# Performance work log

Measured on AMD Instinct MI355X. Metric: run time of the kernel, lower is better.

## Reference

```python
import jax, jax.numpy as jnp
import numpy as np

M0, M1, M2 = 128, 64, 32            # multiplicities of 0e, 1o, 2e
NUM_IRREPS = M0 + M1 + M2           # 224
NODE_DIM = 128
SPH_DIM = M0 + 3 * M1 + 5 * M2      # 480
HIDDEN = 2 * NODE_DIM + NUM_IRREPS  # 480
N = 100000
EPS = 1e-5
SQ3 = float(np.sqrt(3.0))
SQ5 = float(np.sqrt(5.0))


def _split(x):
    s0 = x[:, :M0]                                   # [N,128]   l=0
    s1 = x[:, M0:M0 + 3 * M1].reshape(-1, M1, 3)     # [N,64,3]  l=1
    s2 = x[:, M0 + 3 * M1:].reshape(-1, M2, 5)       # [N,32,5]  l=2
    return s0, s1, s2


def _merge(s0, s1, s2):
    n = s0.shape[0]
    return jnp.concatenate([s0, s1.reshape(n, -1), s2.reshape(n, -1)], axis=-1)


def _o3_linear(s0, s1, s2, w0, w1, w2, b0):
    # e3nn o3.Linear: one path per l, element path-normalization 1/sqrt(mul_in); bias only on 0e
    y0 = s0 @ w0 / np.float32(np.sqrt(M0)) + b0
    y1 = jnp.einsum('nik,io->nok', s1, w1) / np.float32(np.sqrt(M1))
    y2 = jnp.einsum('nik,io->nok', s2, w2) / np.float32(np.sqrt(M2))
    return y0, y1, y2


def _o3_layernorm(s0, s1, s2, w, b):
    # equivariant layer norm: mean-center scalars only; RMS over (mul, components) per irrep type
    f0 = s0 - jnp.mean(s0, axis=1, keepdims=True)
    n0 = jnp.mean(f0 * f0, axis=1, keepdims=True)
    f0 = f0 * jax.lax.rsqrt(n0 + EPS) * w[:M0] + b
    n1 = jnp.mean(s1 * s1, axis=(1, 2))[:, None, None]
    f1 = s1 * jax.lax.rsqrt(n1 + EPS) * w[M0:M0 + M1][None, :, None]
    n2 = jnp.mean(s2 * s2, axis=(1, 2))[:, None, None]
    f2 = s2 * jax.lax.rsqrt(n2 + EPS) * w[M0 + M1:][None, :, None]
    return f0, f1, f2


def setup_inputs() -> dict:
    key = jax.random.key(0)
    ks = jax.random.split(key, 16)
    g = lambda k, shape: jax.random.normal(k, shape, jnp.float32)
    return {
        'x_scalar': g(ks[0], (N, NODE_DIM)),
        'x_spherical': g(ks[1], (N, SPH_DIM)),
        'ln_g': jnp.ones((NODE_DIM,), jnp.float32),
        'ln_b': jnp.zeros((NODE_DIM,), jnp.float32),
        'o3n_w': jnp.ones((NUM_IRREPS,), jnp.float32),
        'o3n_b': jnp.zeros((M0,), jnp.float32),
        'U_w0': g(ks[2], (M0, M0)), 'U_w1': g(ks[3], (M1, M1)), 'U_w2': g(ks[4], (M2, M2)),
        'U_b0': jnp.zeros((M0,), jnp.float32),
        'V_w0': g(ks[5], (M0, M0)), 'V_w1': g(ks[6], (M1, M1)), 'V_w2': g(ks[7], (M2, M2)),
        'V_b0': jnp.zeros((M0,), jnp.float32),
        'dot_w': g(ks[8], (NUM_IRREPS, NODE_DIM)) / np.float32(np.sqrt(NUM_IRREPS)),
        'mlp_w1': g(ks[9], (NODE_DIM + NUM_IRREPS, NODE_DIM)) / np.float32(np.sqrt(NODE_DIM + NUM_IRREPS)),
        'mlp_b1': jnp.zeros((NODE_DIM,), jnp.float32),
        'mlp_w2': g(ks[10], (NODE_DIM, HIDDEN)) / np.float32(np.sqrt(NODE_DIM)),
        'mlp_b2': jnp.zeros((HIDDEN,), jnp.float32),
    }


def reference(x_scalar, x_spherical, ln_g, ln_b, o3n_w, o3n_b,
              U_w0, U_w1, U_w2, U_b0, V_w0, V_w1, V_w2, V_b0,
              dot_w, mlp_w1, mlp_b1, mlp_w2, mlp_b2):
    # scalar layer norm
    mu = jnp.mean(x_scalar, axis=-1, keepdims=True)
    var = jnp.var(x_scalar, axis=-1, keepdims=True)
    scalar_in = (x_scalar - mu) * jax.lax.rsqrt(var + EPS) * ln_g + ln_b
    # equivariant layer norm on spherical features
    s0, s1, s2 = _split(x_spherical)
    s0, s1, s2 = _o3_layernorm(s0, s1, s2, o3n_w, o3n_b)
    U0, U1, U2 = _o3_linear(s0, s1, s2, U_w0, U_w1, U_w2, U_b0)
    V0, V1, V2 = _o3_linear(s0, s1, s2, V_w0, V_w1, V_w2, V_b0)
    # o3.Norm: per-irrep L2 norm -> [N, 224]
    inv = jnp.concatenate([jnp.abs(V0),
                           jnp.sqrt(jnp.sum(V1 * V1, axis=-1)),
                           jnp.sqrt(jnp.sum(V2 * V2, axis=-1))], axis=-1)
    mlp_in = jnp.concatenate([scalar_in, inv], axis=-1)          # [N, 352]
    h = jax.nn.silu(mlp_in @ mlp_w1 + mlp_b1)
    mlp_out = h @ mlp_w2 + mlp_b2                                # [N, 480]
    a_vv = mlp_out[:, :NUM_IRREPS]
    a_sv = mlp_out[:, NUM_IRREPS:NUM_IRREPS + NODE_DIM]
    a_ss = mlp_out[:, NUM_IRREPS + NODE_DIM:]
    # ElementwiseTensorProduct with 224x0e: per-irrep scalar gating (net factor 1)
    d0 = U0 * a_vv[:, :M0]
    d1 = U1 * a_vv[:, M0:M0 + M1, None]
    d2 = U2 * a_vv[:, M0 + M1:, None]
    # EquivariantDot (component-normalized uuu TP to 0e): dot / sqrt(2l+1)
    dot = jnp.concatenate([U0 * V0,
                           jnp.sum(U1 * V1, axis=-1) / SQ3,
                           jnp.sum(U2 * V2, axis=-1) / SQ5], axis=-1)
    inner = dot @ dot_w                                           # [N, 128]
    d_scalar = a_sv * inner + a_ss
    return x_scalar + d_scalar, x_spherical + _merge(d0, d1, d2)
```

## Files before the change

kernel.cpp:

```cpp
#include <hip/hip_runtime.h>
#include <stdint.h>

typedef unsigned short u16;
typedef __attribute__((ext_vector_type(4))) unsigned short u16x4;
typedef __attribute__((ext_vector_type(8))) short s16x8;
typedef __attribute__((ext_vector_type(2))) float f32x2;
typedef __attribute__((ext_vector_type(4))) float f32x4;
typedef __attribute__((ext_vector_type(4), aligned(4))) float f32x4u;

#define NROWS 100000
#define RPB   32
#define NBLK  (NROWS / RPB)
#define NTHR  512

#define PF   488
#define PS   360
#define PH   136
#define PD   232
#define PAB  484
#define PIF  132
#define FIN_RG  (16 * PF)
#define SCB_RG  (16 * PS)
#define HB_RG   (16 * PH)
#define DOT_RG  (16 * PD)
#define AOUT_RG (16 * PAB)
#define INN_RG  (16 * PIF)

#define OFF_FIN   0
#define OFF_AOUT  0
#define OFF_SCB   31232
#define OFF_INNER 31232
#define OFF_DOTB  54272
#define OFF_HB    69120
#define OFF_BCOM  77824
#define ARENA_SZ  79552

#define B_UW0 0
#define B_UW1 16384
#define B_UW2 20480
#define B_VW0 21504
#define B_VW1 37888
#define B_VW2 41984
#define B_DW  43008
#define B_W1  71680
#define B_W2  116736
#define PACK_TOT 178176

__device__ inline float bf2f(u16 u) {
    union { uint32_t i; float f; } v; v.i = (uint32_t)u << 16; return v.f;
}
__device__ inline u16 f2bf(float f) {
    uint32_t d; asm("v_cvt_pk_bf16_f32 %0, %1, %1" : "=v"(d) : "v"(f)); return (u16)d;
}
__device__ inline uint32_t cvtpk(float lo, float hi) {
    uint32_t d; asm("v_cvt_pk_bf16_f32 %0, %1, %2" : "=v"(d) : "v"(lo), "v"(hi)); return d;
}
__device__ inline float wsum32(float v) {
    #pragma unroll
    for (int m = 16; m >= 1; m >>= 1) v += __shfl_xor(v, m);
    return v;
}

struct Ptrs {
    const float *xs, *xp, *lng, *lnb, *o3w, *o3b;
    const float *Uw0, *Uw1, *Uw2, *Ub0, *Vw0, *Vw1, *Vw2, *Vb0;
    const float *dw, *w1, *b1, *w2, *b2;
    const u16 *ws;
    float *out;
};

template<int KS, bool PACKED>
__device__ inline void load_b(const void* W, int D, int tile, int lane, s16x8* bfr)
{
    #pragma unroll
    for (int ks = 0; ks < KS; ++ks) {
        if (PACKED) {
            bfr[ks] = *(const s16x8*)((const u16*)W + (((size_t)tile * KS + ks) * 64 + (size_t)lane) * 8);
        } else {
            union { u16 u[8]; s16x8 v; } bb;
            const int k0 = ks * 32 + ((lane >> 4) << 3), o = tile * 16 + (lane & 15);
            #pragma unroll
            for (int j = 0; j < 8; ++j)
                bb.u[j] = f2bf(((const float*)W)[(size_t)(k0 + j) * D + o]);
            bfr[ks] = bb.v;
        }
    }
}

template<int KS>
__device__ inline f32x4 acc_ab(const u16* A, int pitchA, int lane, const s16x8* bfr)
{
    f32x4 acc = {0.f, 0.f, 0.f, 0.f};
    const u16* arow = A + (lane & 15) * pitchA + (lane >> 4) * 8;
    #pragma unroll
    for (int ks = 0; ks < KS; ++ks) {
        s16x8 a = *(const s16x8*)(arow + ks * 32);
        acc = __builtin_amdgcn_mfma_f32_16x16x32_bf16(a, bfr[ks], acc, 0, 0, 0);
    }
    return acc;
}

__global__ void pack_weights(Ptrs P, u16* ws)
{
    const int gid = blockIdx.x * 256 + threadIdx.x;
    if (gid >= PACK_TOT) return;
    const int  base[10] = {B_UW0, B_UW1, B_UW2, B_VW0, B_VW1, B_VW2, B_DW, B_W1, B_W2, PACK_TOT};
    const int  Kd[9]    = {128, 64, 32, 128, 64, 32, 224, 352, 128};
    const float* srcs[9] = {P.Uw0, P.Uw1, P.Uw2, P.Vw0, P.Vw1, P.Vw2, P.dw, P.w1, P.w2};
    const int  Dstride[9] = {128, 64, 32, 128, 64, 32, 128, 128, 480};
    int m = 0;
    for (int i = 1; i < 9; ++i) if (gid >= base[i]) m = i;
    const int e = gid - base[m];
    const int j = e & 7, lane = (e >> 3) & 63, tk = e >> 9;
    const int Ks = Kd[m] >> 5;
    const int ks = tk % Ks, tile = tk / Ks;
    const int k = ks * 32 + ((lane >> 4) << 3) + j;
    const int o = tile * 16 + (lane & 15);
    ws[gid] = f2bf(srcs[m][(size_t)k * Dstride[m] + o]);
}

__device__ inline void stage1_core(const Ptrs& P, u16* fin0, u16* scb0, int tid, int row0)
{
    const int hw = tid >> 5, l32 = tid & 31;
    #pragma unroll
    for (int rg = 0; rg < 2; ++rg) {
        const int rr = hw + rg * 16;
        const size_t row = (size_t)(row0 + rr);
        u16* finr = fin0 + rg * FIN_RG + hw * PF;
        u16* scbr = scb0 + rg * SCB_RG + hw * PS;
        const float* xsf = P.xs + row * 128;
        const float* xpf = P.xp + row * 480;
        {
            f32x4 u = *(const f32x4*)(xsf + l32 * 4);
            float s  = u[0] + u[1] + u[2] + u[3];
            float s2 = u[0]*u[0] + u[1]*u[1] + u[2]*u[2] + u[3]*u[3];
            s = wsum32(s); s2 = wsum32(s2);
            const float mu = s * (1.f / 128.f);
            const float rs = 1.f / sqrtf(s2 * (1.f / 128.f) - mu * mu + 1e-5f);
            const int c = l32 * 4;
            float t[4];
            #pragma unroll
            for (int j2 = 0; j2 < 4; ++j2)
                t[j2] = (u[j2] - mu) * rs * P.lng[c + j2] + P.lnb[c + j2];
            *(uint32_t*)(scbr + c)     = cvtpk(t[0], t[1]);
            *(uint32_t*)(scbr + c + 2) = cvtpk(t[2], t[3]);
        }
        {
            f32x4 u = *(const f32x4*)(xpf + l32 * 4);
            float s  = u[0] + u[1] + u[2] + u[3];
            float s2 = u[0]*u[0] + u[1]*u[1] + u[2]*u[2] + u[3]*u[3];
            s = wsum32(s); s2 = wsum32(s2);
            const float mu = s * (1.f / 128.f);
            const float rs = 1.f / sqrtf(s2 * (1.f / 128.f) - mu * mu + 1e-5f);
            const int c = l32 * 4;
            float t[4];
            #pragma unroll
            for (int j2 = 0; j2 < 4; ++j2)
                t[j2] = (u[j2] - mu) * rs * P.o3w[c + j2] + P.o3b[c + j2];
            *(uint32_t*)(finr + c)     = cvtpk(t[0], t[1]);
            *(uint32_t*)(finr + c + 2) = cvtpk(t[2], t[3]);
        }
        {
            const int cb = l32 * 6;
            f32x4u a = *(const f32x4u*)(xpf + 128 + cb);
            f32x2  b = *(const f32x2*)(xpf + 128 + cb + 4);
            float w[6] = {a[0], a[1], a[2], a[3], b[0], b[1]};
            float ss = 0.f;
            #pragma unroll
            for (int j2 = 0; j2 < 6; ++j2) ss += w[j2] * w[j2];
            ss = wsum32(ss);
            const float rs = 1.f / sqrtf(ss * (1.f / 192.f) + 1e-5f);
            #pragma unroll
            for (int j2 = 0; j2 < 6; ++j2) {
                const int c = cb + j2, i = c / 3, k = c - 3 * i;
                finr[128 + k * 64 + i] = f2bf(w[j2] * rs * P.o3w[128 + i]);
            }
        }
        {
            const int cb = l32 * 5;
            f32x4u a = *(const f32x4u*)(xpf + 320 + cb);
            float w[5] = {a[0], a[1], a[2], a[3], xpf[320 + cb + 4]};
            float ss = 0.f;
            #pragma unroll
            for (int j2 = 0; j2 < 5; ++j2) ss += w[j2] * w[j2];
            ss = wsum32(ss);
            const float rs = 1.f / sqrtf(ss * (1.f / 160.f) + 1e-5f);
            #pragma unroll
            for (int j2 = 0; j2 < 5; ++j2) {
                const int c = cb + j2, i = c / 5, k = c - 5 * i;
                finr[320 + k * 32 + i] = f2bf(w[j2] * rs * P.o3w[192 + i]);
            }
        }
    }
}

template<bool PACKED>
__global__ __launch_bounds__(NTHR, 4) void xpainn_main(Ptrs P)
{
    __shared__ __align__(16) unsigned char arena[ARENA_SZ];
    u16*   fin    = (u16*)(arena + OFF_FIN);
    u16*   aoutB  = (u16*)(arena + OFF_AOUT);
    u16*   scb    = (u16*)(arena + OFF_SCB);
    float* innerF = (float*)(arena + OFF_INNER);
    u16*   dotb   = (u16*)(arena + OFF_DOTB);
    u16*   hb     = (u16*)(arena + OFF_HB);
    u16*   bcom   = (u16*)(arena + OFF_BCOM);

    const int tid = threadIdx.x;
    const int lane = tid & 63, wave = tid >> 6;
    const int r = lane & 15, g = lane >> 4;
    const int row0 = blockIdx.x * RPB;

    for (int i = tid; i < 864; i += NTHR) {
        const float* src; int off;
        if (i < 128)      { src = P.Ub0; off = i; }
        else if (i < 256) { src = P.Vb0; off = i - 128; }
        else if (i < 384) { src = P.b1;  off = i - 256; }
        else              { src = P.b2;  off = i - 384; }
        bcom[i] = f2bf(src[off]);
    }
    stage1_core(P, fin, scb, tid, row0);
    __syncthreads();

    float u0r[2][4];
    float uxr[2][5][4];
    {
        s16x8 bU[4], bV[4];
        load_b<4, PACKED>(PACKED ? (const void*)(P.ws + B_UW0) : (const void*)P.Uw0, 128, wave, lane, bU);
        load_b<4, PACKED>(PACKED ? (const void*)(P.ws + B_VW0) : (const void*)P.Vw0, 128, wave, lane, bV);
        const int o = wave * 16 + r;
        const float bu = bf2f(bcom[o]), bv = bf2f(bcom[128 + o]);
        #pragma unroll
        for (int rg = 0; rg < 2; ++rg) {
            f32x4 au = acc_ab<4>(fin + rg * FIN_RG, PF, lane, bU);
            f32x4 av = acc_ab<4>(fin + rg * FIN_RG, PF, lane, bV);
            u16* scbR = scb + rg * SCB_RG;
            u16* dotR = dotb + rg * DOT_RG;
            #pragma unroll
            for (int q = 0; q < 4; ++q) {
                const float U = au[q] * 0.08838834764831845f + bu;
                const float V = av[q] * 0.08838834764831845f + bv;
                u0r[rg][q] = U;
                const int lrow = g * 4 + q;
                scbR[lrow * PS + 128 + o] = f2bf(fabsf(V));
                dotR[lrow * PD + o]       = f2bf(U * V);
            }
        }
    }
    if (wave < 4) {
        const int tt = wave, o = tt * 16 + r;
        float sv[2][4] = {{0.f,0.f,0.f,0.f},{0.f,0.f,0.f,0.f}};
        float suv[2][4] = {{0.f,0.f,0.f,0.f},{0.f,0.f,0.f,0.f}};
        #pragma unroll
        for (int ch = 0; ch < 3; ++ch) {
            s16x8 bU[2], bV[2];
            load_b<2, PACKED>(PACKED ? (const void*)(P.ws + B_UW1) : (const void*)P.Uw1, 64, tt, lane, bU);
            load_b<2, PACKED>(PACKED ? (const void*)(P.ws + B_VW1) : (const void*)P.Vw1, 64, tt, lane, bV);
            #pragma unroll
            for (int rg = 0; rg < 2; ++rg) {
                f32x4 au = acc_ab<2>(fin + rg * FIN_RG + 128 + 64 * ch, PF, lane, bU);
                f32x4 av = acc_ab<2>(fin + rg * FIN_RG + 128 + 64 * ch, PF, lane, bV);
                #pragma unroll
                for (int q = 0; q < 4; ++q) {
                    const float U = au[q] * 0.125f, V = av[q] * 0.125f;
                    uxr[rg][ch][q] = U; sv[rg][q] += V * V; suv[rg][q] += U * V;
                }
            }
        }
        #pragma unroll
        for (int rg = 0; rg < 2; ++rg) {
            #pragma unroll
            for (int q = 0; q < 4; ++q) {
                const int lrow = g * 4 + q;
                (scb + rg * SCB_RG)[lrow * PS + 256 + o]  = f2bf(sqrtf(sv[rg][q]));
                (dotb + rg * DOT_RG)[lrow * PD + 128 + o] = f2bf(suv[rg][q] * 0.5773502691896258f);
            }
        }
    } else if (wave < 6) {
        const int tt = wave - 4, o = tt * 16 + r;
        float sv[2][4] = {{0.f,0.f,0.f,0.f},{0.f,0.f,0.f,0.f}};
        float suv[2][4] = {{0.f,0.f,0.f,0.f},{0.f,0.f,0.f,0.f}};
        #pragma unroll
        for (int ch = 0; ch < 5; ++ch) {
            s16x8 bU[1], bV[1];
            load_b<1, PACKED>(PACKED ? (const void*)(P.ws + B_UW2) : (const void*)P.Uw2, 32, tt, lane, bU);
            load_b<1, PACKED>(PACKED ? (const void*)(P.ws + B_VW2) : (const void*)P.Vw2, 32, tt, lane, bV);
            #pragma unroll
            for (int rg = 0; rg < 2; ++rg) {
                f32x4 au = acc_ab<1>(fin + rg * FIN_RG + 320 + 32 * ch, PF, lane, bU);
                f32x4 av = acc_ab<1>(fin + rg * FIN_RG + 320 + 32 * ch, PF, lane, bV);
                #pragma unroll
                for (int q = 0; q < 4; ++q) {
                    const float U = au[q] * 0.17677669529663687f, V = av[q] * 0.17677669529663687f;
                    uxr[rg][ch][q] = U; sv[rg][q] += V * V; suv[rg][q] += U * V;
                }
            }
        }
        #pragma unroll
        for (int rg = 0; rg < 2; ++rg) {
            #pragma unroll
            for (int q = 0; q < 4; ++q) {
                const int lrow = g * 4 + q;
                (scb + rg * SCB_RG)[lrow * PS + 320 + o]  = f2bf(sqrtf(sv[rg][q]));
                (dotb + rg * DOT_RG)[lrow * PD + 192 + o] = f2bf(suv[rg][q] * 0.4472135954999579f);
            }
        }
    }
    __syncthreads();

    #pragma unroll
    for (int rg = 0; rg < 2; ++rg) {
        s16x8 bfr[11];
        load_b<11, PACKED>(PACKED ? (const void*)(P.ws + B_W1) : (const void*)P.w1, 128, wave, lane, bfr);
        f32x4 acc = acc_ab<11>(scb + rg * SCB_RG, PS, lane, bfr);
        const int o = wave * 16 + r;
        const float bv = bf2f(bcom[256 + o]);
        #pragma unroll
        for (int q = 0; q < 4; ++q) {
            float x = acc[q] + bv;
            hb[rg * HB_RG + (g * 4 + q) * PH + o] = f2bf(x / (1.f + expf(-x)));
        }
    }
    __syncthreads();

    {
        float avv0[2][4], avv1[2][4];
        {
            s16x8 bfr[4];
            load_b<4, PACKED>(PACKED ? (const void*)(P.ws + B_W2) : (const void*)P.w2, 480, wave, lane, bfr);
            const int o = wave * 16 + r;
            const float bv = bf2f(bcom[384 + o]);
            #pragma unroll
            for (int rg = 0; rg < 2; ++rg) {
                f32x4 acc = acc_ab<4>(hb + rg * HB_RG, PH, lane, bfr);
                #pragma unroll
                for (int q = 0; q < 4; ++q) avv0[rg][q] = acc[q] + bv;
            }
        }
        {
            const int ti = wave + 8;
            s16x8 bfr[4];
            load_b<4, PACKED>(PACKED ? (const void*)(P.ws + B_W2) : (const void*)P.w2, 480, ti, lane, bfr);
            const int o = ti * 16 + r;
            const float bv = bf2f(bcom[384 + o]);
            #pragma unroll
            for (int rg = 0; rg < 2; ++rg) {
                f32x4 acc = acc_ab<4>(hb + rg * HB_RG, PH, lane, bfr);
                if (wave < 6) {
                    #pragma unroll
                    for (int q = 0; q < 4; ++q) avv1[rg][q] = acc[q] + bv;
                } else {
                    u16* aoutR = aoutB + rg * AOUT_RG;
                    #pragma unroll
                    for (int q = 0; q < 4; ++q)
                        aoutR[(g * 4 + q) * PAB + o] = f2bf(acc[q] + bv);
                }
            }
        }
        {
            const size_t ob = (size_t)NROWS * 128;
            #pragma unroll
            for (int rg = 0; rg < 2; ++rg) {
                const int o = wave * 16 + r;
                #pragma unroll
                for (int q = 0; q < 4; ++q) {
                    const size_t gr = (size_t)(row0 + rg * 16 + g * 4 + q) * 480;
                    P.out[ob + gr + o] = P.xp[gr + o] + u0r[rg][q] * avv0[rg][q];
                }
                if (wave < 4) {
                    const int i = wave * 16 + r;
                    #pragma unroll
                    for (int q = 0; q < 4; ++q) {
                        const size_t gr = (size_t)(row0 + rg * 16 + g * 4 + q) * 480;
                        #pragma unroll
                        for (int ch = 0; ch < 3; ++ch) {
                            const size_t c = 128 + 3 * i + ch;
                            P.out[ob + gr + c] = P.xp[gr + c] + uxr[rg][ch][q] * avv1[rg][q];
                        }
                    }
                } else if (wave < 6) {
                    const int i = (wave - 4) * 16 + r;
                    #pragma unroll
                    for (int q = 0; q < 4; ++q) {
                        const size_t gr = (size_t)(row0 + rg * 16 + g * 4 + q) * 480;
                        #pragma unroll
                        for (int ch = 0; ch < 5; ++ch) {
                            const size_t c = 320 + 5 * i + ch;
                            P.out[ob + gr + c] = P.xp[gr + c] + uxr[rg][ch][q] * avv1[rg][q];
                        }
                    }
                }
            }
        }
        for (int ti = wave + 16; ti < 38; ti += 8) {
            if (ti < 30) {
                s16x8 bfr[4];
                load_b<4, PACKED>(PACKED ? (const void*)(P.ws + B_W2) : (const void*)P.w2, 480, ti, lane, bfr);
                const int o = ti * 16 + r;
                const float bv = bf2f(bcom[384 + o]);
                #pragma unroll
                for (int rg = 0; rg < 2; ++rg) {
                    f32x4 acc = acc_ab<4>(hb + rg * HB_RG, PH, lane, bfr);
                    u16* aoutR = aoutB + rg * AOUT_RG;
                    #pragma unroll
                    for (int q = 0; q < 4; ++q)
                        aoutR[(g * 4 + q) * PAB + o] = f2bf(acc[q] + bv);
                }
            } else {
                s16x8 bfr[7];
                load_b<7, PACKED>(PACKED ? (const void*)(P.ws + B_DW) : (const void*)P.dw, 128, ti - 30, lane, bfr);
                const int oo = (ti - 30) * 16 + r;
                #pragma unroll
                for (int rg = 0; rg < 2; ++rg) {
                    f32x4 acc = acc_ab<7>(dotb + rg * DOT_RG, PD, lane, bfr);
                    float* innR = innerF + rg * INN_RG;
                    #pragma unroll
                    for (int q = 0; q < 4; ++q)
                        innR[(g * 4 + q) * PIF + oo] = acc[q];
                }
            }
        }
    }
    __syncthreads();

    #pragma unroll
    for (int it = 0; it < 2; ++it) {
        const int idx = tid + it * NTHR;
        const int r2 = idx >> 5, c4 = (idx & 31) * 4;
        const u16*  aoutR = aoutB + (r2 >> 4) * AOUT_RG + (r2 & 15) * PAB;
        const float* innR = innerF + (r2 >> 4) * INN_RG + (r2 & 15) * PIF;
        const size_t gb = (size_t)(row0 + r2) * 128 + c4;
        const u16x4 asv = *(const u16x4*)(aoutR + 224 + c4);
        const u16x4 ass = *(const u16x4*)(aoutR + 352 + c4);
        const f32x4 inn = *(const f32x4*)(innR + c4);
        const f32x4 xs = *(const f32x4*)(P.xs + gb);
        f32x4 o;
        #pragma unroll
        for (int j = 0; j < 4; ++j) o[j] = xs[j] + bf2f(asv[j]) * inn[j] + bf2f(ass[j]);
        *(f32x4*)(P.out + gb) = o;
    }
}

extern "C" void kernel_launch(void* const* d_in, const int* in_sizes, int n_in,
                              void* d_out, int out_size, void* d_ws, size_t ws_size,
                              hipStream_t stream)
{
    Ptrs P;
    P.xs  = (const float*)d_in[0];  P.xp  = (const float*)d_in[1];
    P.lng = (const float*)d_in[2];  P.lnb = (const float*)d_in[3];
    P.o3w = (const float*)d_in[4];  P.o3b = (const float*)d_in[5];
    P.Uw0 = (const float*)d_in[6];  P.Uw1 = (const float*)d_in[7];
    P.Uw2 = (const float*)d_in[8];  P.Ub0 = (const float*)d_in[9];
    P.Vw0 = (const float*)d_in[10]; P.Vw1 = (const float*)d_in[11];
    P.Vw2 = (const float*)d_in[12]; P.Vb0 = (const float*)d_in[13];
    P.dw  = (const float*)d_in[14]; P.w1  = (const float*)d_in[15];
    P.b1  = (const float*)d_in[16]; P.w2  = (const float*)d_in[17];
    P.b2  = (const float*)d_in[18];
    P.ws  = (const u16*)d_ws;
    P.out = (float*)d_out;

    const bool packed = (ws_size >= (size_t)PACK_TOT * sizeof(u16));
    if (packed) {
        pack_weights<<<(PACK_TOT + 255) / 256, 256, 0, stream>>>(P, (u16*)d_ws);
        xpainn_main<true><<<NBLK, NTHR, 0, stream>>>(P);
    } else {
        xpainn_main<false><<<NBLK, NTHR, 0, stream>>>(P);
    }
}
```

Before: 220.3 us.

## Double block to 1024 threads and redistribute per-stage work across 16 waves

```diff
diff --git a/kernel.cpp b/kernel.cpp
--- a/kernel.cpp
+++ b/kernel.cpp
@@ -11,7 +11,7 @@
 #define NROWS 100000
 #define RPB   32
 #define NBLK  (NROWS / RPB)
-#define NTHR  512
+#define NTHR  1024
 
 #define PF   488
 #define PS   360
@@ -121,81 +121,77 @@
 
 __device__ inline void stage1_core(const Ptrs& P, u16* fin0, u16* scb0, int tid, int row0)
 {
-    const int hw = tid >> 5, l32 = tid & 31;
-    #pragma unroll
-    for (int rg = 0; rg < 2; ++rg) {
-        const int rr = hw + rg * 16;
-        const size_t row = (size_t)(row0 + rr);
-        u16* finr = fin0 + rg * FIN_RG + hw * PF;
-        u16* scbr = scb0 + rg * SCB_RG + hw * PS;
-        const float* xsf = P.xs + row * 128;
-        const float* xpf = P.xp + row * 480;
-        {
-            f32x4 u = *(const f32x4*)(xsf + l32 * 4);
-            float s  = u[0] + u[1] + u[2] + u[3];
-            float s2 = u[0]*u[0] + u[1]*u[1] + u[2]*u[2] + u[3]*u[3];
-            s = wsum32(s); s2 = wsum32(s2);
-            const float mu = s * (1.f / 128.f);
-            const float rs = 1.f / sqrtf(s2 * (1.f / 128.f) - mu * mu + 1e-5f);
-            const int c = l32 * 4;
-            float t[4];
-            #pragma unroll
-            for (int j2 = 0; j2 < 4; ++j2)
-                t[j2] = (u[j2] - mu) * rs * P.lng[c + j2] + P.lnb[c + j2];
-            *(uint32_t*)(scbr + c)     = cvtpk(t[0], t[1]);
-            *(uint32_t*)(scbr + c + 2) = cvtpk(t[2], t[3]);
-        }
-        {
-            f32x4 u = *(const f32x4*)(xpf + l32 * 4);
-            float s  = u[0] + u[1] + u[2] + u[3];
-            float s2 = u[0]*u[0] + u[1]*u[1] + u[2]*u[2] + u[3]*u[3];
-            s = wsum32(s); s2 = wsum32(s2);
-            const float mu = s * (1.f / 128.f);
-            const float rs = 1.f / sqrtf(s2 * (1.f / 128.f) - mu * mu + 1e-5f);
-            const int c = l32 * 4;
-            float t[4];
-            #pragma unroll
-            for (int j2 = 0; j2 < 4; ++j2)
-                t[j2] = (u[j2] - mu) * rs * P.o3w[c + j2] + P.o3b[c + j2];
-            *(uint32_t*)(finr + c)     = cvtpk(t[0], t[1]);
-            *(uint32_t*)(finr + c + 2) = cvtpk(t[2], t[3]);
-        }
-        {
-            const int cb = l32 * 6;
-            f32x4u a = *(const f32x4u*)(xpf + 128 + cb);
-            f32x2  b = *(const f32x2*)(xpf + 128 + cb + 4);
-            float w[6] = {a[0], a[1], a[2], a[3], b[0], b[1]};
-            float ss = 0.f;
-            #pragma unroll
-            for (int j2 = 0; j2 < 6; ++j2) ss += w[j2] * w[j2];
-            ss = wsum32(ss);
-            const float rs = 1.f / sqrtf(ss * (1.f / 192.f) + 1e-5f);
-            #pragma unroll
-            for (int j2 = 0; j2 < 6; ++j2) {
-                const int c = cb + j2, i = c / 3, k = c - 3 * i;
-                finr[128 + k * 64 + i] = f2bf(w[j2] * rs * P.o3w[128 + i]);
-            }
-        }
-        {
-            const int cb = l32 * 5;
-            f32x4u a = *(const f32x4u*)(xpf + 320 + cb);
-            float w[5] = {a[0], a[1], a[2], a[3], xpf[320 + cb + 4]};
-            float ss = 0.f;
-            #pragma unroll
-            for (int j2 = 0; j2 < 5; ++j2) ss += w[j2] * w[j2];
-            ss = wsum32(ss);
-            const float rs = 1.f / sqrtf(ss * (1.f / 160.f) + 1e-5f);
-            #pragma unroll
-            for (int j2 = 0; j2 < 5; ++j2) {
-                const int c = cb + j2, i = c / 5, k = c - 5 * i;
-                finr[320 + k * 32 + i] = f2bf(w[j2] * rs * P.o3w[192 + i]);
-            }
+    const int rr = tid >> 5, l32 = tid & 31;
+    const size_t row = (size_t)(row0 + rr);
+    u16* finr = fin0 + (rr >> 4) * FIN_RG + (rr & 15) * PF;
+    u16* scbr = scb0 + (rr >> 4) * SCB_RG + (rr & 15) * PS;
+    const float* xsf = P.xs + row * 128;
+    const float* xpf = P.xp + row * 480;
+    {
+        f32x4 u = *(const f32x4*)(xsf + l32 * 4);
+        float s  = u[0] + u[1] + u[2] + u[3];
+        float s2 = u[0]*u[0] + u[1]*u[1] + u[2]*u[2] + u[3]*u[3];
+        s = wsum32(s); s2 = wsum32(s2);
+        const float mu = s * (1.f / 128.f);
+        const float rs = 1.f / sqrtf(s2 * (1.f / 128.f) - mu * mu + 1e-5f);
+        const int c = l32 * 4;
+        float t[4];
+        #pragma unroll
+        for (int j2 = 0; j2 < 4; ++j2)
+            t[j2] = (u[j2] - mu) * rs * P.lng[c + j2] + P.lnb[c + j2];
+        *(uint32_t*)(scbr + c)     = cvtpk(t[0], t[1]);
+        *(uint32_t*)(scbr + c + 2) = cvtpk(t[2], t[3]);
+    }
+    {
+        f32x4 u = *(const f32x4*)(xpf + l32 * 4);
+        float s  = u[0] + u[1] + u[2] + u[3];
+        float s2 = u[0]*u[0] + u[1]*u[1] + u[2]*u[2] + u[3]*u[3];
+        s = wsum32(s); s2 = wsum32(s2);
+        const float mu = s * (1.f / 128.f);
+        const float rs = 1.f / sqrtf(s2 * (1.f / 128.f) - mu * mu + 1e-5f);
+        const int c = l32 * 4;
+        float t[4];
+        #pragma unroll
+        for (int j2 = 0; j2 < 4; ++j2)
+            t[j2] = (u[j2] - mu) * rs * P.o3w[c + j2] + P.o3b[c + j2];
+        *(uint32_t*)(finr + c)     = cvtpk(t[0], t[1]);
+        *(uint32_t*)(finr + c + 2) = cvtpk(t[2], t[3]);
+    }
+    {
+        const int cb = l32 * 6;
+        f32x4u a = *(const f32x4u*)(xpf + 128 + cb);
+        f32x2  b = *(const f32x2*)(xpf + 128 + cb + 4);
+        float w[6] = {a[0], a[1], a[2], a[3], b[0], b[1]};
+        float ss = 0.f;
+        #pragma unroll
+        for (int j2 = 0; j2 < 6; ++j2) ss += w[j2] * w[j2];
+        ss = wsum32(ss);
+        const float rs = 1.f / sqrtf(ss * (1.f / 192.f) + 1e-5f);
+        #pragma unroll
+        for (int j2 = 0; j2 < 6; ++j2) {
+            const int c = cb + j2, i = c / 3, k = c - 3 * i;
+            finr[128 + k * 64 + i] = f2bf(w[j2] * rs * P.o3w[128 + i]);
+        }
+    }
+    {
+        const int cb = l32 * 5;
+        f32x4u a = *(const f32x4u*)(xpf + 320 + cb);
+        float w[5] = {a[0], a[1], a[2], a[3], xpf[320 + cb + 4]};
+        float ss = 0.f;
+        #pragma unroll
+        for (int j2 = 0; j2 < 5; ++j2) ss += w[j2] * w[j2];
+        ss = wsum32(ss);
+        const float rs = 1.f / sqrtf(ss * (1.f / 160.f) + 1e-5f);
+        #pragma unroll
+        for (int j2 = 0; j2 < 5; ++j2) {
+            const int c = cb + j2, i = c / 5, k = c - 5 * i;
+            finr[320 + k * 32 + i] = f2bf(w[j2] * rs * P.o3w[192 + i]);
         }
     }
 }
 
 template<bool PACKED>
-__global__ __launch_bounds__(NTHR, 4) void xpainn_main(Ptrs P)
+__global__ __launch_bounds__(NTHR) void xpainn_main(Ptrs P)
 {
     __shared__ __align__(16) unsigned char arena[ARENA_SZ];
     u16*   fin    = (u16*)(arena + OFF_FIN);
@@ -224,7 +220,7 @@
 
     float u0r[2][4];
     float uxr[2][5][4];
-    {
+    if (wave < 8) {
         s16x8 bU[4], bV[4];
         load_b<4, PACKED>(PACKED ? (const void*)(P.ws + B_UW0) : (const void*)P.Uw0, 128, wave, lane, bU);
         load_b<4, PACKED>(PACKED ? (const void*)(P.ws + B_VW0) : (const void*)P.Vw0, 128, wave, lane, bV);
@@ -246,9 +242,8 @@
                 dotR[lrow * PD + o]       = f2bf(U * V);
             }
         }
-    }
-    if (wave < 4) {
-        const int tt = wave, o = tt * 16 + r;
+    } else if (wave < 12) {
+        const int tt = wave - 8, o = tt * 16 + r;
         float sv[2][4] = {{0.f,0.f,0.f,0.f},{0.f,0.f,0.f,0.f}};
         float suv[2][4] = {{0.f,0.f,0.f,0.f},{0.f,0.f,0.f,0.f}};
         #pragma unroll
@@ -276,8 +271,8 @@
                 (dotb + rg * DOT_RG)[lrow * PD + 128 + o] = f2bf(suv[rg][q] * 0.5773502691896258f);
             }
         }
-    } else if (wave < 6) {
-        const int tt = wave - 4, o = tt * 16 + r;
+    } else if (wave < 14) {
+        const int tt = wave - 12, o = tt * 16 + r;
         float sv[2][4] = {{0.f,0.f,0.f,0.f},{0.f,0.f,0.f,0.f}};
         float suv[2][4] = {{0.f,0.f,0.f,0.f},{0.f,0.f,0.f,0.f}};
         #pragma unroll
@@ -308,12 +303,12 @@
     }
     __syncthreads();
 
-    #pragma unroll
-    for (int rg = 0; rg < 2; ++rg) {
+    {
+        const int tile = wave & 7, rg = wave >> 3;
         s16x8 bfr[11];
-        load_b<11, PACKED>(PACKED ? (const void*)(P.ws + B_W1) : (const void*)P.w1, 128, wave, lane, bfr);
+        load_b<11, PACKED>(PACKED ? (const void*)(P.ws + B_W1) : (const void*)P.w1, 128, tile, lane, bfr);
         f32x4 acc = acc_ab<11>(scb + rg * SCB_RG, PS, lane, bfr);
-        const int o = wave * 16 + r;
+        const int o = tile * 16 + r;
         const float bv = bf2f(bcom[256 + o]);
         #pragma unroll
         for (int q = 0; q < 4; ++q) {
@@ -323,22 +318,73 @@
     }
     __syncthreads();
 
-    {
-        float avv0[2][4], avv1[2][4];
-        {
-            s16x8 bfr[4];
-            load_b<4, PACKED>(PACKED ? (const void*)(P.ws + B_W2) : (const void*)P.w2, 480, wave, lane, bfr);
-            const int o = wave * 16 + r;
-            const float bv = bf2f(bcom[384 + o]);
-            #pragma unroll
-            for (int rg = 0; rg < 2; ++rg) {
-                f32x4 acc = acc_ab<4>(hb + rg * HB_RG, PH, lane, bfr);
-                #pragma unroll
-                for (int q = 0; q < 4; ++q) avv0[rg][q] = acc[q] + bv;
-            }
-        }
-        {
-            const int ti = wave + 8;
+    if (wave < 8) {
+        s16x8 bfr[4];
+        load_b<4, PACKED>(PACKED ? (const void*)(P.ws + B_W2) : (const void*)P.w2, 480, wave, lane, bfr);
+        const int o = wave * 16 + r;
+        const float bv = bf2f(bcom[384 + o]);
+        const size_t ob = (size_t)NROWS * 128;
+        #pragma unroll
+        for (int rg = 0; rg < 2; ++rg) {
+            f32x4 acc = acc_ab<4>(hb + rg * HB_RG, PH, lane, bfr);
+            #pragma unroll
+            for (int q = 0; q < 4; ++q) {
+                const float avv0 = acc[q] + bv;
+                const size_t gr = (size_t)(row0 + rg * 16 + g * 4 + q) * 480;
+                P.out[ob + gr + o] = P.xp[gr + o] + u0r[rg][q] * avv0;
+            }
+        }
+    } else if (wave < 14) {
+        s16x8 bfr[4];
+        load_b<4, PACKED>(PACKED ? (const void*)(P.ws + B_W2) : (const void*)P.w2, 480, wave, lane, bfr);
+        const float bv = bf2f(bcom[384 + wave * 16 + r]);
+        const size_t ob = (size_t)NROWS * 128;
+        #pragma unroll
+        for (int rg = 0; rg < 2; ++rg) {
+            f32x4 acc = acc_ab<4>(hb + rg * HB_RG, PH, lane, bfr);
+            if (wave < 12) {
+                const int i = (wave - 8) * 16 + r;
+                #pragma unroll
+                for (int q = 0; q < 4; ++q) {
+                    const float avv1 = acc[q] + bv;
+                    const size_t gr = (size_t)(row0 + rg * 16 + g * 4 + q) * 480;
+                    #pragma unroll
+                    for (int ch = 0; ch < 3; ++ch) {
+                        const size_t c = 128 + 3 * i + ch;
+                        P.out[ob + gr + c] = P.xp[gr + c] + uxr[rg][ch][q] * avv1;
+                    }
+                }
+            } else {
+                const int i = (wave - 12) * 16 + r;
+                #pragma unroll
+                for (int q = 0; q < 4; ++q) {
+                    const float avv1 = acc[q] + bv;
+                    const size_t gr = (size_t)(row0 + rg * 16 + g * 4 + q) * 480;
+                    #pragma unroll
+                    for (int ch = 0; ch < 5; ++ch) {
+                        const size_t c = 320 + 5 * i + ch;
+                        P.out[ob + gr + c] = P.xp[gr + c] + uxr[rg][ch][q] * avv1;
+                    }
+                }
+            }
+        }
+    } else {
+        s16x8 bfr[4];
+        load_b<4, PACKED>(PACKED ? (const void*)(P.ws + B_W2) : (const void*)P.w2, 480, wave, lane, bfr);
+        const int o = wave * 16 + r;
+        const float bv = bf2f(bcom[384 + o]);
+        #pragma unroll
+        for (int rg = 0; rg < 2; ++rg) {
+            f32x4 acc = acc_ab<4>(hb + rg * HB_RG, PH, lane, bfr);
+            u16* aoutR = aoutB + rg * AOUT_RG;
+            #pragma unroll
+            for (int q = 0; q < 4; ++q)
+                aoutR[(g * 4 + q) * PAB + o] = f2bf(acc[q] + bv);
+        }
+    }
+    for (int tt = wave; tt < 22; tt += 16) {
+        if (tt < 14) {
+            const int ti = 16 + tt;
             s16x8 bfr[4];
             load_b<4, PACKED>(PACKED ? (const void*)(P.ws + B_W2) : (const void*)P.w2, 480, ti, lane, bfr);
             const int o = ti * 16 + r;
@@ -346,87 +392,30 @@
             #pragma unroll
             for (int rg = 0; rg < 2; ++rg) {
                 f32x4 acc = acc_ab<4>(hb + rg * HB_RG, PH, lane, bfr);
-                if (wave < 6) {
-                    #pragma unroll
-                    for (int q = 0; q < 4; ++q) avv1[rg][q] = acc[q] + bv;
-                } else {
-                    u16* aoutR = aoutB + rg * AOUT_RG;
-                    #pragma unroll
-                    for (int q = 0; q < 4; ++q)
-                        aoutR[(g * 4 + q) * PAB + o] = f2bf(acc[q] + bv);
-                }
-            }
-        }
-        {
-            const size_t ob = (size_t)NROWS * 128;
+                u16* aoutR = aoutB + rg * AOUT_RG;
+                #pragma unroll
+                for (int q = 0; q < 4; ++q)
+                    aoutR[(g * 4 + q) * PAB + o] = f2bf(acc[q] + bv);
+            }
+        } else {
+            const int ti = tt - 14;
+            s16x8 bfr[7];
+            load_b<7, PACKED>(PACKED ? (const void*)(P.ws + B_DW) : (const void*)P.dw, 128, ti, lane, bfr);
+            const int oo = ti * 16 + r;
             #pragma unroll
             for (int rg = 0; rg < 2; ++rg) {
-                const int o = wave * 16 + r;
-                #pragma unroll
-                for (int q = 0; q < 4; ++q) {
-                    const size_t gr = (size_t)(row0 + rg * 16 + g * 4 + q) * 480;
-                    P.out[ob + gr + o] = P.xp[gr + o] + u0r[rg][q] * avv0[rg][q];
-                }
-                if (wave < 4) {
-                    const int i = wave * 16 + r;
-                    #pragma unroll
-                    for (int q = 0; q < 4; ++q) {
-                        const size_t gr = (size_t)(row0 + rg * 16 + g * 4 + q) * 480;
-                        #pragma unroll
-                        for (int ch = 0; ch < 3; ++ch) {
-                            const size_t c = 128 + 3 * i + ch;
-                            P.out[ob + gr + c] = P.xp[gr + c] + uxr[rg][ch][q] * avv1[rg][q];
-                        }
-                    }
-                } else if (wave < 6) {
-                    const int i = (wave - 4) * 16 + r;
-                    #pragma unroll
-                    for (int q = 0; q < 4; ++q) {
-                        const size_t gr = (size_t)(row0 + rg * 16 + g * 4 + q) * 480;
-                        #pragma unroll
-                        for (int ch = 0; ch < 5; ++ch) {
-                            const size_t c = 320 + 5 * i + ch;
-                            P.out[ob + gr + c] = P.xp[gr + c] + uxr[rg][ch][q] * avv1[rg][q];
-                        }
-                    }
-                }
-            }
-        }
-        for (int ti = wave + 16; ti < 38; ti += 8) {
-            if (ti < 30) {
-                s16x8 bfr[4];
-                load_b<4, PACKED>(PACKED ? (const void*)(P.ws + B_W2) : (const void*)P.w2, 480, ti, lane, bfr);
-                const int o = ti * 16 + r;
-                const float bv = bf2f(bcom[384 + o]);
-                #pragma unroll
-                for (int rg = 0; rg < 2; ++rg) {
-                    f32x4 acc = acc_ab<4>(hb + rg * HB_RG, PH, lane, bfr);
-                    u16* aoutR = aoutB + rg * AOUT_RG;
-                    #pragma unroll
-                    for (int q = 0; q < 4; ++q)
-                        aoutR[(g * 4 + q) * PAB + o] = f2bf(acc[q] + bv);
-                }
-            } else {
-                s16x8 bfr[7];
-                load_b<7, PACKED>(PACKED ? (const void*)(P.ws + B_DW) : (const void*)P.dw, 128, ti - 30, lane, bfr);
-                const int oo = (ti - 30) * 16 + r;
-                #pragma unroll
-                for (int rg = 0; rg < 2; ++rg) {
-                    f32x4 acc = acc_ab<7>(dotb + rg * DOT_RG, PD, lane, bfr);
-                    float* innR = innerF + rg * INN_RG;
-                    #pragma unroll
-                    for (int q = 0; q < 4; ++q)
-                        innR[(g * 4 + q) * PIF + oo] = acc[q];
-                }
+                f32x4 acc = acc_ab<7>(dotb + rg * DOT_RG, PD, lane, bfr);
+                float* innR = innerF + rg * INN_RG;
+                #pragma unroll
+                for (int q = 0; q < 4; ++q)
+                    innR[(g * 4 + q) * PIF + oo] = acc[q];
             }
         }
     }
     __syncthreads();
 
-    #pragma unroll
-    for (int it = 0; it < 2; ++it) {
-        const int idx = tid + it * NTHR;
-        const int r2 = idx >> 5, c4 = (idx & 31) * 4;
+    {
+        const int r2 = tid >> 5, c4 = (tid & 31) * 4;
         const u16*  aoutR = aoutB + (r2 >> 4) * AOUT_RG + (r2 & 15) * PAB;
         const float* innR = innerF + (r2 >> 4) * INN_RG + (r2 & 15) * PIF;
         const size_t gb = (size_t)(row0 + r2) * 128 + c4;
```

After: 260.0 us. 18.0% more time.
